# Performance work log

Measured on AMD Instinct MI355X. Metric: run time of the kernel, lower is better.

## Reference

```python
import jax, jax.numpy as jnp
import numpy as np

B, S = 256, 256          # batch, seq_len
V, E = 8000, 128         # char vocab, char emb dim
HC, HW = 128, 256        # char_lstm_hid_dim, word_lstm_hid_dim


def setup_inputs() -> dict:
    key = jax.random.key(0)
    ks = jax.random.split(key, 20)
    n = lambda k, sh: (jax.random.normal(k, sh) * 0.05).astype(jnp.float32)
    return {
        "insts": jax.random.randint(ks[0], (B, S), 0, V),
        "golds": jax.random.randint(ks[1], (B, S), 0, 3),
        "emb": n(ks[2], (V, E)),
        "Wih_f": n(ks[3], (4 * HC, E)), "Whh_f": n(ks[4], (4 * HC, HC)), "b_f": n(ks[5], (4 * HC,)),
        "Wih_b": n(ks[6], (4 * HC, E)), "Whh_b": n(ks[7], (4 * HC, HC)), "b_b": n(ks[8], (4 * HC,)),
        "sub_Wih": n(ks[9], (4 * HW, 2 * HC)), "sub_Whh": n(ks[10], (4 * HW, HW)), "sub_b": n(ks[11], (4 * HW,)),
        "wrd_Wih": n(ks[12], (4 * HW, HW)), "wrd_Whh": n(ks[13], (4 * HW, HW)), "wrd_b": n(ks[14], (4 * HW,)),
        "cls_W": n(ks[15], (2, HW + 2 * HC)), "cls_b": n(ks[16], (2,)),
    }


def _cell(x, h, c, Wih, Whh, b):
    # PyTorch LSTMCell convention: gates ordered i, f, g, o
    g = x @ Wih.T + h @ Whh.T + b
    i, f, gg, o = jnp.split(g, 4, axis=-1)
    c = jax.nn.sigmoid(f) * c + jax.nn.sigmoid(i) * jnp.tanh(gg)
    h = jax.nn.sigmoid(o) * jnp.tanh(c)
    return h, c


def reference(insts, golds, emb, Wih_f, Whh_f, b_f, Wih_b, Whh_b, b_b,
              sub_Wih, sub_Whh, sub_b, wrd_Wih, wrd_Whh, wrd_b, cls_W, cls_b):
    # --- CharEncoder: embedding + BiLSTM, seq-first output [S, B, 2*HC] ---
    x = emb[insts].transpose(1, 0, 2)  # [S, B, E]
    z = jnp.zeros((B, HC), x.dtype)

    def mk_step(Wih, Whh, b):
        def step(hc, xt):
            h, c = _cell(xt, hc[0], hc[1], Wih, Whh, b)
            return (h, c), h
        return step

    _, hf = jax.lax.scan(mk_step(Wih_f, Whh_f, b_f), (z, z), x)
    _, hb = jax.lax.scan(mk_step(Wih_b, Whh_b, b_b), (z, z), x[::-1])
    chars = jnp.concatenate([hf, hb[::-1]], axis=-1)  # [S, B, 2*HC]

    # subword LSTM input at step t is chars[t-1] (zeros at t=0)
    sub_in = jnp.concatenate([jnp.zeros((1, B, 2 * HC), chars.dtype), chars[:-1]], axis=0)

    smap = jnp.array([1, 2, 2], jnp.int32)  # subword_action_map
    wmap = jnp.array([0, 1, 1], jnp.int32)  # word_action_map
    bidx = jnp.arange(B)

    # stacks: read state at pos, write new state at pos+1, then pos += op
    sh = jnp.zeros((2 * S + 2, B, HW), chars.dtype)
    sc = jnp.zeros((2 * S + 2, B, HW), chars.dtype)
    wh = jnp.zeros((S + 1, B, HW), chars.dtype)
    wc = jnp.zeros((S + 1, B, HW), chars.dtype)
    sp = jnp.zeros((B,), jnp.int32)
    wp = jnp.zeros((B,), jnp.int32)

    def step(carry, inp):
        sh, sc, sp, wh, wc, wp = carry
        xs, xc, g = inp  # subword input [B,2HC], classifier char feat [B,2HC], gold op [B]
        h1, c1 = _cell(xs, sh[sp, bidx], sc[sp, bidx], sub_Wih, sub_Whh, sub_b)
        sh = sh.at[sp + 1, bidx].set(h1)
        sc = sc.at[sp + 1, bidx].set(c1)
        h2, c2 = _cell(h1, wh[wp, bidx], wc[wp, bidx], wrd_Wih, wrd_Whh, wrd_b)
        wh = wh.at[wp + 1, bidx].set(h2)
        wc = wc.at[wp + 1, bidx].set(c2)
        out = jnp.concatenate([h2, xc], axis=-1) @ cls_W.T + cls_b  # [B, 2]
        return (sh, sc, sp + smap[g], wh, wc, wp + wmap[g]), out

    _, outs = jax.lax.scan(step, (sh, sc, sp, wh, wc, wp),
                           (sub_in, chars, golds.T.astype(jnp.int32)))
    return outs.transpose(1, 0, 2)  # [B, S, 2]
```

## Files before the change

kernel.cpp:

```cpp
#include <hip/hip_runtime.h>

#define S_LEN 256
#define BATCH 256

typedef _Float16 f16;
typedef _Float16 f16x8 __attribute__((ext_vector_type(8)));
typedef _Float16 f16x4 __attribute__((ext_vector_type(4)));
typedef float f32x4 __attribute__((ext_vector_type(4)));
typedef unsigned u32x4 __attribute__((ext_vector_type(4)));

__device__ inline float sigf(float x) { return 1.f / (1.f + __expf(-x)); }
__device__ inline float tanhf2(float x) { return 2.f * sigf(2.f * x) - 1.f; }

#define BARRIER_LGKM() asm volatile("s_waitcnt lgkmcnt(0)\n\ts_barrier" ::: "memory")

__global__ void k_convert(const float* __restrict__ w3, const float* __restrict__ w4,
                          const float* __restrict__ w6, const float* __restrict__ w7,
                          const float* __restrict__ w9, const float* __restrict__ w10,
                          const float* __restrict__ w12, const float* __restrict__ w13,
                          f16* __restrict__ dst) {
  int i = blockIdx.x * blockDim.x + threadIdx.x;
  const int n = 1310720;
  for (; i < n; i += gridDim.x * blockDim.x) {
    float v;
    if (i < 262144) {
      int m = i >> 16, j = i & 65535;
      v = (m == 0 ? w3 : m == 1 ? w4 : m == 2 ? w6 : w7)[j];
    } else {
      int k = i - 262144;
      int m = k >> 18, j = k & 262143;
      v = (m == 0 ? w9 : m == 1 ? w10 : m == 2 ? w12 : w13)[j];
    }
    dst[i] = (f16)v;
  }
}

__global__ void k_zero(unsigned* __restrict__ p, int n) {
  int i = blockIdx.x * blockDim.x + threadIdx.x;
  for (; i < n; i += gridDim.x * blockDim.x) p[i] = 0u;
}

__global__ void k_gather(const int* __restrict__ insts, const float* __restrict__ emb,
                         f16* __restrict__ Xf) {
  int gid = blockIdx.x * blockDim.x + threadIdx.x;
  int row = gid >> 5;
  int ch = gid & 31;
  int t = row >> 8, b = row & 255;
  int v = insts[b * S_LEN + t];
  const float* src = emb + (size_t)v * 128 + ch * 4;
  f16x4 d;
  d[0] = (f16)src[0]; d[1] = (f16)src[1]; d[2] = (f16)src[2]; d[3] = (f16)src[3];
  *(f16x4*)&Xf[(size_t)row * 128 + ch * 4] = d;
}

__global__ __launch_bounds__(256)
void k_gih_char(const f16* __restrict__ wbuf, const float* __restrict__ bias_f,
                const float* __restrict__ bias_b, const f16* __restrict__ Xf,
                f16* __restrict__ gih, int sbase) {
  const int team = blockIdx.x & 15;
  const int tc = (blockIdx.x >> 4) & 3;
  const int gc = (blockIdx.x >> 6) & 1;
  const int dr = blockIdx.x >> 7;
  const int m0 = team * 16;
  const f16* Wih = wbuf + (dr ? 131072 : 0);
  const float* bias = dr ? bias_b : bias_f;
  const int lane = threadIdx.x & 63, wave = threadIdx.x >> 6;
  const int l15 = lane & 15, kb = (lane >> 4) * 8;
  const int rbase = gc * 256 + wave * 64;

  f16x8 fw[4][4];
  float bv[4];
#pragma unroll
  for (int tt = 0; tt < 4; ++tt) {
    int col = rbase + tt * 16 + l15;
    bv[tt] = bias[col];
#pragma unroll
    for (int ks = 0; ks < 4; ++ks)
      fw[tt][ks] = *(const f16x8*)&Wih[col * 128 + ks * 32 + kb];
  }

  for (int st = 0; st < 16; ++st) {
    const int srel = tc * 16 + st;
    const int s = sbase + srel;
    const int t_in = dr ? (255 - s) : s;
    f32x4 acc[4];
#pragma unroll
    for (int tt = 0; tt < 4; ++tt) { f32x4 a = {bv[tt], bv[tt], bv[tt], bv[tt]}; acc[tt] = a; }
    f16x8 ax[4];
#pragma unroll
    for (int ks = 0; ks < 4; ++ks)
      ax[ks] = *(const f16x8*)&Xf[(size_t)t_in * BATCH * 128 + (m0 + l15) * 128 + ks * 32 + kb];
#pragma unroll
    for (int ks = 0; ks < 4; ++ks)
#pragma unroll
      for (int tt = 0; tt < 4; ++tt)
        acc[tt] = __builtin_amdgcn_mfma_f32_16x16x32_f16(ax[ks], fw[tt][ks], acc[tt], 0, 0, 0);
#pragma unroll
    for (int tt = 0; tt < 4; ++tt) {
      f16x4 o;
#pragma unroll
      for (int r = 0; r < 4; ++r) o[r] = (f16)acc[tt][r];
      size_t off = ((((size_t)dr * 16 + team) * 64 + srel) * 512 + rbase + tt * 16 + l15) * 16 +
                   (lane >> 4) * 4;
      *(f16x4*)&gih[off] = o;
    }
  }
}

__global__ __launch_bounds__(512)
void k_chain_char(const f16* __restrict__ wbuf, const f16* __restrict__ gih,
                  f16* __restrict__ chars, float* __restrict__ c_save, int sbase) {
  const int dr = blockIdx.x >> 4;
  const int teamc = blockIdx.x & 15;
  const f16* Whh = wbuf + (dr ? 196608 : 65536);
  const int tid = threadIdx.x, lane = tid & 63, wave = tid >> 6;
  const int l15 = lane & 15, kb = (lane >> 4) * 8;
  const int u0 = wave * 16;
  const int bq = lane >> 4;
  const int cbase = dr ? 128 : 0;

  __shared__ f16 hs[2][16][136];

  f16x8 fh[4][4];
#pragma unroll
  for (int g = 0; g < 4; ++g)
#pragma unroll
    for (int ks = 0; ks < 4; ++ks)
      fh[g][ks] = *(const f16x8*)&Whh[(g * 128 + u0 + l15) * 128 + ks * 32 + kb];

  float c[4];
  const size_t csoff = (((size_t)dr * 16 + teamc) * 128 + u0 + l15) * 16 + bq * 4;
  if (sbase) {
#pragma unroll
    for (int r = 0; r < 4; ++r) c[r] = c_save[csoff + r];
    const int t_prev = dr ? (256 - sbase) : (sbase - 1);
    int b = tid >> 5, u4 = (tid & 31) * 4;
    *(f16x4*)&hs[0][b][u4] =
        *(const f16x4*)&chars[((size_t)(teamc * 256 + t_prev) * 16 + b) * 256 + cbase + u4];
  } else {
#pragma unroll
    for (int r = 0; r < 4; ++r) c[r] = 0.f;
    int b = tid >> 5, u4 = (tid & 31) * 4;
    f16x4 z = {};
    *(f16x4*)&hs[0][b][u4] = z;
  }
  __syncthreads();

  const f16* gbase = gih + (((size_t)dr * 16 + teamc) * 64) * 512 * 16;
  f16x4 gcur[4], gnext[4];
#pragma unroll
  for (int g = 0; g < 4; ++g)
    gcur[g] = *(const f16x4*)&gbase[((size_t)0 * 512 + g * 128 + u0 + l15) * 16 + bq * 4];
  int par = 0;
  for (int st = 0; st < 64; ++st) {
    const int s = sbase + st;
    if (st < 63) {
#pragma unroll
      for (int g = 0; g < 4; ++g)
        gnext[g] =
            *(const f16x4*)&gbase[((size_t)(st + 1) * 512 + g * 128 + u0 + l15) * 16 + bq * 4];
    }
    f16x8 ah[4];
#pragma unroll
    for (int ks = 0; ks < 4; ++ks) ah[ks] = *(const f16x8*)&hs[par][l15][ks * 32 + kb];
    f32x4 acc[4];
#pragma unroll
    for (int g = 0; g < 4; ++g) {
      f32x4 a = {(float)gcur[g][0], (float)gcur[g][1], (float)gcur[g][2], (float)gcur[g][3]};
      acc[g] = a;
    }
#pragma unroll
    for (int ks = 0; ks < 4; ++ks)
#pragma unroll
      for (int g = 0; g < 4; ++g)
        acc[g] = __builtin_amdgcn_mfma_f32_16x16x32_f16(ah[ks], fh[g][ks], acc[g], 0, 0, 0);
    const int t_out = dr ? (255 - s) : s;
#pragma unroll
    for (int r = 0; r < 4; ++r) {
      float cc = sigf(acc[1][r]) * c[r] + sigf(acc[0][r]) * tanhf2(acc[2][r]);
      c[r] = cc;
      f16 hv = (f16)(sigf(acc[3][r]) * tanhf2(cc));
      int b = bq * 4 + r;
      chars[((size_t)(teamc * 256 + t_out) * 16 + b) * 256 + cbase + u0 + l15] = hv;
      hs[par ^ 1][b][u0 + l15] = hv;
    }
#pragma unroll
    for (int g = 0; g < 4; ++g) gcur[g] = gnext[g];
    par ^= 1;
    BARRIER_LGKM();
  }
#pragma unroll
  for (int r = 0; r < 4; ++r) c_save[csoff + r] = c[r];
}

__global__ __launch_bounds__(256, 1)
void k_subword(const f16* __restrict__ wbuf, const f16* __restrict__ chars,
               const int* __restrict__ golds,
               const float* __restrict__ b_sub, const float* __restrict__ b_wrd,
               unsigned* __restrict__ pub, unsigned* __restrict__ flags,
               f16* __restrict__ H2) {
  const int team = blockIdx.x >> 4;
  const int q = blockIdx.x & 15;
  const int m0 = team * 16;
  const int h0 = q * 16;
  const int tid = threadIdx.x, lane = tid & 63, wave = tid >> 6;
  const int l15 = lane & 15, kb = (lane >> 4) * 8;

  const f16* sWih = wbuf + 262144;
  const f16* sWhh = wbuf + 524288;
  const f16* wWih = wbuf + 786432;
  const f16* wWhh = wbuf + 1048576;

  __shared__ f16 xs_s[16][264];
  __shared__ f16 h1_s[16][264];
  __shared__ f16 wh_s[16][264];
  __shared__ float gexS[16][68];
  __shared__ float gexW[16][68];
  __shared__ int golds_s[16][256];

  f32x4 fsi[8], fsh[8], fwi[8], fwh[8];
  const int wr = wave * 256 + h0 + l15;
#pragma unroll
  for (int ks = 0; ks < 8; ++ks) {
    fsi[ks] = *(const volatile f32x4*)&sWih[wr * 256 + ks * 32 + kb];
    fsh[ks] = *(const volatile f32x4*)&sWhh[wr * 256 + ks * 32 + kb];
    fwi[ks] = *(const volatile f32x4*)&wWih[wr * 256 + ks * 32 + kb];
    fwh[ks] = *(const volatile f32x4*)&wWhh[wr * 256 + ks * 32 + kb];
  }
  const float bS = b_sub[wr], bW = b_wrd[wr];

  for (int i = tid; i < 16 * 256; i += 256)
    golds_s[i >> 8][i & 255] = golds[(m0 + (i >> 8)) * S_LEN + (i & 255)];
  for (int i = tid; i < 16 * 264; i += 256) {
    ((f16*)xs_s)[i] = (f16)0.f;
    ((f16*)h1_s)[i] = (f16)0.f;
    ((f16*)wh_s)[i] = (f16)0.f;
  }
  const int cm = tid >> 4, cj = tid & 15;
  const int sr = tid >> 4;
  const int sc = (tid & 15) * 16;
  float c_sub = 0.f, c_wrd = 0.f, wh_reg = 0.f;
  __syncthreads();

  for (int i = 0; i <= S_LEN; ++i) {
    const bool doW = (i > 0), doS = (i < S_LEN);
    const int slotbase = ((i & 1) * 16 + team) << 12;

    f16x4 chpre[4];
    if (doS) {
#pragma unroll
      for (int p = 0; p < 4; ++p)
        chpre[p] = *(const f16x4*)&chars[(size_t)(((team * S_LEN + i) * 16 + sr) * 256) +
                                         sc + p * 4];
    }

    f32x4 accW = {bW, bW, bW, bW};
    f32x4 accS = {bS, bS, bS, bS};
    if (doW) {
#pragma unroll
      for (int ks = 0; ks < 8; ++ks) {
        f16x8 a1 = *(const f16x8*)&h1_s[l15][ks * 32 + kb];
        f16x8 aw = *(const f16x8*)&wh_s[l15][ks * 32 + kb];
        accW = __builtin_amdgcn_mfma_f32_16x16x32_f16(
            a1, __builtin_bit_cast(f16x8, fwi[ks]), accW, 0, 0, 0);
        accW = __builtin_amdgcn_mfma_f32_16x16x32_f16(
            aw, __builtin_bit_cast(f16x8, fwh[ks]), accW, 0, 0, 0);
      }
    }
    if (doS) {
      const bool keep = (i > 0) && (golds_s[l15][i > 0 ? i - 1 : 0] == 0);
      f16x8 z8 = {};
#pragma unroll
      for (int ks = 0; ks < 8; ++ks) {
        f16x8 axv = *(const f16x8*)&xs_s[l15][ks * 32 + kb];
        f16x8 a1 = *(const f16x8*)&h1_s[l15][ks * 32 + kb];
        a1 = keep ? a1 : z8;
        accS = __builtin_amdgcn_mfma_f32_16x16x32_f16(
            axv, __builtin_bit_cast(f16x8, fsi[ks]), accS, 0, 0, 0);
        accS = __builtin_amdgcn_mfma_f32_16x16x32_f16(
            a1, __builtin_bit_cast(f16x8, fsh[ks]), accS, 0, 0, 0);
      }
    }
#pragma unroll
    for (int r = 0; r < 4; ++r) {
      if (doW) gexW[(lane >> 4) * 4 + r][wave * 16 + l15] = accW[r];
      if (doS) gexS[(lane >> 4) * 4 + r][wave * 16 + l15] = accS[r];
    }
    __syncthreads();

    const int gprev = (i > 0) ? golds_s[cm][i - 1] : 1;
    if (doW) {
      float gi = gexW[cm][cj], gf = gexW[cm][16 + cj], gg = gexW[cm][32 + cj],
            go = gexW[cm][48 + cj];
      float c2 = sigf(gf) * c_wrd + sigf(gi) * tanhf2(gg);
      float h2 = sigf(go) * tanhf2(c2);
      bool adv = (gprev != 0);
      if (adv) { c_wrd = c2; wh_reg = h2; }
      H2[(size_t)(i - 1) * BATCH * 256 + (m0 + cm) * 256 + h0 + cj] = (f16)h2;
    }
    if (doS) {
      float gi = gexS[cm][cj], gf = gexS[cm][16 + cj], gg = gexS[cm][32 + cj],
            go = gexS[cm][48 + cj];
      float cp = (gprev == 0) ? c_sub : 0.f;
      float c1 = sigf(gf) * cp + sigf(gi) * tanhf2(gg);
      c_sub = c1;
      f16 h1 = (f16)(sigf(go) * tanhf2(c1));
      unsigned val = ((unsigned)__builtin_bit_cast(unsigned short, h1) << 16) |
                     (unsigned)__builtin_bit_cast(unsigned short, (f16)wh_reg);
      __hip_atomic_store(&pub[slotbase + cm * 256 + h0 + cj], val, __ATOMIC_RELAXED,
                         __HIP_MEMORY_SCOPE_AGENT);
    }
    __syncthreads();

    if (doS) {
      if (tid == 0)
        __hip_atomic_store(&flags[(team * 16 + q) * 16], (unsigned)(i + 1), __ATOMIC_RELAXED,
                           __HIP_MEMORY_SCOPE_AGENT);
      if (tid < 64) {
        const unsigned tgt = (unsigned)(i + 1);
        while (true) {
          unsigned v = tgt;
          if (lane < 16)
            v = __hip_atomic_load(&flags[(team * 16 + lane) * 16], __ATOMIC_RELAXED,
                                  __HIP_MEMORY_SCOPE_AGENT);
          if (__all(v >= tgt)) break;
          __builtin_amdgcn_s_sleep(1);
        }
      }
      asm volatile("" ::: "memory");
      __syncthreads();
      u32x4 w0, w1, w2, w3;
      {
        const unsigned* pb = &pub[slotbase + sr * 256 + sc];
        asm volatile(
            "global_load_dwordx4 %0, %4, off sc0 sc1\n\t"
            "global_load_dwordx4 %1, %5, off sc0 sc1\n\t"
            "global_load_dwordx4 %2, %6, off sc0 sc1\n\t"
            "global_load_dwordx4 %3, %7, off sc0 sc1\n\t"
            "s_waitcnt vmcnt(0)"
            : "=&v"(w0), "=&v"(w1), "=&v"(w2), "=&v"(w3)
            : "v"(pb), "v"(pb + 4), "v"(pb + 8), "v"(pb + 12));
      }
      union { unsigned short s[8]; f16x8 v; } uh0, uw0, uh1, uw1;
#pragma unroll
      for (int k = 0; k < 4; ++k) {
        uh0.s[k] = (unsigned short)(w0[k] >> 16);
        uw0.s[k] = (unsigned short)(w0[k] & 0xffffu);
        uh0.s[4 + k] = (unsigned short)(w1[k] >> 16);
        uw0.s[4 + k] = (unsigned short)(w1[k] & 0xffffu);
        uh1.s[k] = (unsigned short)(w2[k] >> 16);
        uw1.s[k] = (unsigned short)(w2[k] & 0xffffu);
        uh1.s[4 + k] = (unsigned short)(w3[k] >> 16);
        uw1.s[4 + k] = (unsigned short)(w3[k] & 0xffffu);
      }
      *(f16x8*)&h1_s[sr][sc] = uh0.v;
      *(f16x8*)&wh_s[sr][sc] = uw0.v;
      *(f16x8*)&h1_s[sr][sc + 8] = uh1.v;
      *(f16x8*)&wh_s[sr][sc + 8] = uw1.v;
#pragma unroll
      for (int p = 0; p < 4; ++p) *(f16x4*)&xs_s[sr][sc + p * 4] = chpre[p];
      __syncthreads();
    }
  }
}

__global__ __launch_bounds__(256)
void k_cls(const f16* __restrict__ H2, const f16* __restrict__ chars,
           const float* __restrict__ clsW, const float* __restrict__ clsb,
           float* __restrict__ out) {
  const int w = (blockIdx.x << 2) | (threadIdx.x >> 6);
  const int lane = threadIdx.x & 63;
  const int t = w >> 8, b = w & 255;
  const f16* h2p = H2 + (size_t)w * 256;
  const f16* chp = chars + (size_t)(((b >> 4) * S_LEN + t) * 16 + (b & 15)) * 256;
  float s0 = 0.f, s1 = 0.f;
  f16x4 hv = *(const f16x4*)&h2p[lane * 4];
  f16x4 cv = *(const f16x4*)&chp[lane * 4];
#pragma unroll
  for (int qq = 0; qq < 4; ++qq) {
    int u = lane * 4 + qq;
    s0 += (float)hv[qq] * clsW[u] + (float)cv[qq] * clsW[256 + u];
    s1 += (float)hv[qq] * clsW[512 + u] + (float)cv[qq] * clsW[768 + u];
  }
#pragma unroll
  for (int off = 32; off >= 1; off >>= 1) {
    s0 += __shfl_down(s0, off);
    s1 += __shfl_down(s1, off);
  }
  if (lane == 0) {
    out[((size_t)b * S_LEN + t) * 2 + 0] = s0 + clsb[0];
    out[((size_t)b * S_LEN + t) * 2 + 1] = s1 + clsb[1];
  }
}

extern "C" void kernel_launch(void* const* d_in, const int* in_sizes, int n_in,
                              void* d_out, int out_size, void* d_ws, size_t ws_size,
                              hipStream_t stream) {
  const int* insts = (const int*)d_in[0];
  const int* golds = (const int*)d_in[1];
  const float* emb = (const float*)d_in[2];
  const float* wihf = (const float*)d_in[3];
  const float* whhf = (const float*)d_in[4];
  const float* bf = (const float*)d_in[5];
  const float* wihb = (const float*)d_in[6];
  const float* whhb = (const float*)d_in[7];
  const float* bb = (const float*)d_in[8];
  const float* swih = (const float*)d_in[9];
  const float* swhh = (const float*)d_in[10];
  const float* sb = (const float*)d_in[11];
  const float* wwih = (const float*)d_in[12];
  const float* wwhh = (const float*)d_in[13];
  const float* wb = (const float*)d_in[14];
  const float* clsW = (const float*)d_in[15];
  const float* clsb = (const float*)d_in[16];
  float* out = (float*)d_out;

  const size_t OFF_W = 0;
  const size_t OFF_XF = 2621440;
  const size_t OFF_PUB = OFF_XF + 4194304;
  const size_t OFF_FLAGS = OFF_PUB + 524288;
  const size_t OFF_CHARS = 19398656;
  const size_t OFF_A = 52953088;
  const size_t OFF_TAIL = 86507520;
  const size_t TOTAL = 87048192;
  if (ws_size < TOTAL) return;

  char* ws = (char*)d_ws;
  f16* wbuf = (f16*)(ws + OFF_W);
  f16* Xf = (f16*)(ws + OFF_XF);
  f16* chars = (f16*)(ws + OFF_CHARS);
  f16* gih = (f16*)(ws + OFF_A);
  f16* H2 = (f16*)(ws + OFF_A);
  float* c_save = (float*)(ws + OFF_TAIL);
  unsigned* pub = (unsigned*)(ws + OFF_PUB);
  unsigned* flags = (unsigned*)(ws + OFF_FLAGS);

  hipLaunchKernelGGL(k_convert, dim3(1024), dim3(256), 0, stream, wihf, whhf, wihb, whhb,
                     swih, swhh, wwih, wwhh, wbuf);
  hipLaunchKernelGGL(k_gather, dim3(8192), dim3(256), 0, stream, insts, emb, Xf);

  for (int sb4 = 0; sb4 < 256; sb4 += 64) {
    hipLaunchKernelGGL(k_gih_char, dim3(256), dim3(256), 0, stream, wbuf, bf, bb, Xf, gih,
                       sb4);
    hipLaunchKernelGGL(k_chain_char, dim3(32), dim3(512), 0, stream, wbuf, gih, chars,
                       c_save, sb4);
  }

  hipLaunchKernelGGL(k_zero, dim3(16), dim3(256), 0, stream, (unsigned*)(ws + OFF_FLAGS),
                     4096);
  hipLaunchKernelGGL(k_subword, dim3(256), dim3(256), 0, stream, wbuf, chars, golds, sb, wb,
                     pub, flags, H2);
  hipLaunchKernelGGL(k_cls, dim3(16384), dim3(256), 0, stream, H2, chars, clsW, clsb, out);
}
```

Before: 1.370 ms.

## Fuse char input projection into recurrent char LSTM kernel

Replaces the chunked pair of kernels (a separate input-projection GEMM writing gih to global memory, then a recurrent chain reading it back) with one kernel that keeps both Wih and Whh fragments in registers. Each step computes the next timestep's input projection from Xf while the current recurrence runs. This removes the 8 launches, the gih round trip through global memory and the c_save/h reload between chunks. The trade-off is extra MFMA work and register pressure on the serial critical path of only 32 blocks.

```diff
diff --git a/kernel.cpp b/kernel.cpp
--- a/kernel.cpp
+++ b/kernel.cpp
@@ -53,66 +53,16 @@
   *(f16x4*)&Xf[(size_t)row * 128 + ch * 4] = d;
 }
 
-__global__ __launch_bounds__(256)
-void k_gih_char(const f16* __restrict__ wbuf, const float* __restrict__ bias_f,
-                const float* __restrict__ bias_b, const f16* __restrict__ Xf,
-                f16* __restrict__ gih, int sbase) {
-  const int team = blockIdx.x & 15;
-  const int tc = (blockIdx.x >> 4) & 3;
-  const int gc = (blockIdx.x >> 6) & 1;
-  const int dr = blockIdx.x >> 7;
-  const int m0 = team * 16;
-  const f16* Wih = wbuf + (dr ? 131072 : 0);
-  const float* bias = dr ? bias_b : bias_f;
-  const int lane = threadIdx.x & 63, wave = threadIdx.x >> 6;
-  const int l15 = lane & 15, kb = (lane >> 4) * 8;
-  const int rbase = gc * 256 + wave * 64;
-
-  f16x8 fw[4][4];
-  float bv[4];
-#pragma unroll
-  for (int tt = 0; tt < 4; ++tt) {
-    int col = rbase + tt * 16 + l15;
-    bv[tt] = bias[col];
-#pragma unroll
-    for (int ks = 0; ks < 4; ++ks)
-      fw[tt][ks] = *(const f16x8*)&Wih[col * 128 + ks * 32 + kb];
-  }
-
-  for (int st = 0; st < 16; ++st) {
-    const int srel = tc * 16 + st;
-    const int s = sbase + srel;
-    const int t_in = dr ? (255 - s) : s;
-    f32x4 acc[4];
-#pragma unroll
-    for (int tt = 0; tt < 4; ++tt) { f32x4 a = {bv[tt], bv[tt], bv[tt], bv[tt]}; acc[tt] = a; }
-    f16x8 ax[4];
-#pragma unroll
-    for (int ks = 0; ks < 4; ++ks)
-      ax[ks] = *(const f16x8*)&Xf[(size_t)t_in * BATCH * 128 + (m0 + l15) * 128 + ks * 32 + kb];
-#pragma unroll
-    for (int ks = 0; ks < 4; ++ks)
-#pragma unroll
-      for (int tt = 0; tt < 4; ++tt)
-        acc[tt] = __builtin_amdgcn_mfma_f32_16x16x32_f16(ax[ks], fw[tt][ks], acc[tt], 0, 0, 0);
-#pragma unroll
-    for (int tt = 0; tt < 4; ++tt) {
-      f16x4 o;
-#pragma unroll
-      for (int r = 0; r < 4; ++r) o[r] = (f16)acc[tt][r];
-      size_t off = ((((size_t)dr * 16 + team) * 64 + srel) * 512 + rbase + tt * 16 + l15) * 16 +
-                   (lane >> 4) * 4;
-      *(f16x4*)&gih[off] = o;
-    }
-  }
-}
-
-__global__ __launch_bounds__(512)
-void k_chain_char(const f16* __restrict__ wbuf, const f16* __restrict__ gih,
-                  f16* __restrict__ chars, float* __restrict__ c_save, int sbase) {
+__global__ __launch_bounds__(512, 2)
+void k_char_fused(const f16* __restrict__ wbuf, const float* __restrict__ bias_f,
+                  const float* __restrict__ bias_b, const f16* __restrict__ Xf,
+                  f16* __restrict__ chars) {
   const int dr = blockIdx.x >> 4;
   const int teamc = blockIdx.x & 15;
+  const int m0 = teamc * 16;
+  const f16* Wih = wbuf + (dr ? 131072 : 0);
   const f16* Whh = wbuf + (dr ? 196608 : 65536);
+  const float* bias = dr ? bias_b : bias_f;
   const int tid = threadIdx.x, lane = tid & 63, wave = tid >> 6;
   const int l15 = lane & 15, kb = (lane >> 4) * 8;
   const int u0 = wave * 16;
@@ -121,60 +71,67 @@
 
   __shared__ f16 hs[2][16][136];
 
-  f16x8 fh[4][4];
-#pragma unroll
-  for (int g = 0; g < 4; ++g)
-#pragma unroll
-    for (int ks = 0; ks < 4; ++ks)
-      fh[g][ks] = *(const f16x8*)&Whh[(g * 128 + u0 + l15) * 128 + ks * 32 + kb];
-
-  float c[4];
-  const size_t csoff = (((size_t)dr * 16 + teamc) * 128 + u0 + l15) * 16 + bq * 4;
-  if (sbase) {
-#pragma unroll
-    for (int r = 0; r < 4; ++r) c[r] = c_save[csoff + r];
-    const int t_prev = dr ? (256 - sbase) : (sbase - 1);
-    int b = tid >> 5, u4 = (tid & 31) * 4;
-    *(f16x4*)&hs[0][b][u4] =
-        *(const f16x4*)&chars[((size_t)(teamc * 256 + t_prev) * 16 + b) * 256 + cbase + u4];
-  } else {
-#pragma unroll
-    for (int r = 0; r < 4; ++r) c[r] = 0.f;
+  f16x8 fw[4][4], fh[4][4];
+  float bv[4];
+#pragma unroll
+  for (int g = 0; g < 4; ++g) {
+    const int row = g * 128 + u0 + l15;
+    bv[g] = bias[row];
+#pragma unroll
+    for (int ks = 0; ks < 4; ++ks) {
+      fw[g][ks] = *(const f16x8*)&Wih[row * 128 + ks * 32 + kb];
+      fh[g][ks] = *(const f16x8*)&Whh[row * 128 + ks * 32 + kb];
+    }
+  }
+
+  float c[4] = {0.f, 0.f, 0.f, 0.f};
+  {
     int b = tid >> 5, u4 = (tid & 31) * 4;
     f16x4 z = {};
     *(f16x4*)&hs[0][b][u4] = z;
   }
   __syncthreads();
 
-  const f16* gbase = gih + (((size_t)dr * 16 + teamc) * 64) * 512 * 16;
-  f16x4 gcur[4], gnext[4];
-#pragma unroll
-  for (int g = 0; g < 4; ++g)
-    gcur[g] = *(const f16x4*)&gbase[((size_t)0 * 512 + g * 128 + u0 + l15) * 16 + bq * 4];
+  f32x4 gacc[4];
+  {
+    const int t0 = dr ? 255 : 0;
+    f16x8 ax[4];
+#pragma unroll
+    for (int ks = 0; ks < 4; ++ks)
+      ax[ks] = *(const f16x8*)&Xf[(size_t)t0 * BATCH * 128 + (m0 + l15) * 128 + ks * 32 + kb];
+#pragma unroll
+    for (int g = 0; g < 4; ++g) { f32x4 a = {bv[g], bv[g], bv[g], bv[g]}; gacc[g] = a; }
+#pragma unroll
+    for (int ks = 0; ks < 4; ++ks)
+#pragma unroll
+      for (int g = 0; g < 4; ++g)
+        gacc[g] = __builtin_amdgcn_mfma_f32_16x16x32_f16(ax[ks], fw[g][ks], gacc[g], 0, 0, 0);
+  }
+
   int par = 0;
-  for (int st = 0; st < 64; ++st) {
-    const int s = sbase + st;
-    if (st < 63) {
-#pragma unroll
-      for (int g = 0; g < 4; ++g)
-        gnext[g] =
-            *(const f16x4*)&gbase[((size_t)(st + 1) * 512 + g * 128 + u0 + l15) * 16 + bq * 4];
-    }
+  for (int st = 0; st < 256; ++st) {
+    f16x8 axn[4];
+    if (st < 255) {
+      const int tn = dr ? (254 - st) : (st + 1);
+#pragma unroll
+      for (int ks = 0; ks < 4; ++ks)
+        axn[ks] =
+            *(const f16x8*)&Xf[(size_t)tn * BATCH * 128 + (m0 + l15) * 128 + ks * 32 + kb];
+    }
+
     f16x8 ah[4];
 #pragma unroll
     for (int ks = 0; ks < 4; ++ks) ah[ks] = *(const f16x8*)&hs[par][l15][ks * 32 + kb];
     f32x4 acc[4];
 #pragma unroll
-    for (int g = 0; g < 4; ++g) {
-      f32x4 a = {(float)gcur[g][0], (float)gcur[g][1], (float)gcur[g][2], (float)gcur[g][3]};
-      acc[g] = a;
-    }
+    for (int g = 0; g < 4; ++g) acc[g] = gacc[g];
 #pragma unroll
     for (int ks = 0; ks < 4; ++ks)
 #pragma unroll
       for (int g = 0; g < 4; ++g)
         acc[g] = __builtin_amdgcn_mfma_f32_16x16x32_f16(ah[ks], fh[g][ks], acc[g], 0, 0, 0);
-    const int t_out = dr ? (255 - s) : s;
+
+    const int t_out = dr ? (255 - st) : st;
 #pragma unroll
     for (int r = 0; r < 4; ++r) {
       float cc = sigf(acc[1][r]) * c[r] + sigf(acc[0][r]) * tanhf2(acc[2][r]);
@@ -184,13 +141,20 @@
       chars[((size_t)(teamc * 256 + t_out) * 16 + b) * 256 + cbase + u0 + l15] = hv;
       hs[par ^ 1][b][u0 + l15] = hv;
     }
-#pragma unroll
-    for (int g = 0; g < 4; ++g) gcur[g] = gnext[g];
+
+    if (st < 255) {
+#pragma unroll
+      for (int g = 0; g < 4; ++g) { f32x4 a = {bv[g], bv[g], bv[g], bv[g]}; gacc[g] = a; }
+#pragma unroll
+      for (int ks = 0; ks < 4; ++ks)
+#pragma unroll
+        for (int g = 0; g < 4; ++g)
+          gacc[g] =
+              __builtin_amdgcn_mfma_f32_16x16x32_f16(axn[ks], fw[g][ks], gacc[g], 0, 0, 0);
+    }
     par ^= 1;
     BARRIER_LGKM();
   }
-#pragma unroll
-  for (int r = 0; r < 4; ++r) c_save[csoff + r] = c[r];
 }
 
 __global__ __launch_bounds__(256, 1)
@@ -421,7 +385,6 @@
   const size_t OFF_FLAGS = OFF_PUB + 524288;
   const size_t OFF_CHARS = 19398656;
   const size_t OFF_A = 52953088;
-  const size_t OFF_TAIL = 86507520;
   const size_t TOTAL = 87048192;
   if (ws_size < TOTAL) return;
 
@@ -429,9 +392,7 @@
   f16* wbuf = (f16*)(ws + OFF_W);
   f16* Xf = (f16*)(ws + OFF_XF);
   f16* chars = (f16*)(ws + OFF_CHARS);
-  f16* gih = (f16*)(ws + OFF_A);
   f16* H2 = (f16*)(ws + OFF_A);
-  float* c_save = (float*)(ws + OFF_TAIL);
   unsigned* pub = (unsigned*)(ws + OFF_PUB);
   unsigned* flags = (unsigned*)(ws + OFF_FLAGS);
 
@@ -439,12 +400,7 @@
                      swih, swhh, wwih, wwhh, wbuf);
   hipLaunchKernelGGL(k_gather, dim3(8192), dim3(256), 0, stream, insts, emb, Xf);
 
-  for (int sb4 = 0; sb4 < 256; sb4 += 64) {
-    hipLaunchKernelGGL(k_gih_char, dim3(256), dim3(256), 0, stream, wbuf, bf, bb, Xf, gih,
-                       sb4);
-    hipLaunchKernelGGL(k_chain_char, dim3(32), dim3(512), 0, stream, wbuf, gih, chars,
-                       c_save, sb4);
-  }
+  hipLaunchKernelGGL(k_char_fused, dim3(32), dim3(512), 0, stream, wbuf, bf, bb, Xf, chars);
 
   hipLaunchKernelGGL(k_zero, dim3(16), dim3(256), 0, stream, (unsigned*)(ws + OFF_FLAGS),
                      4096);
```

Measured after the change: 1.303 ms. -4.9%, faster.
